# Kernel tuning notes

Hardware: AMD Instinct MI355X
Metric: run time of the kernel (lower is better)

The kernel has to match this reference:

```python
import jax, jax.numpy as jnp
import numpy as np

N_ATOMS = 128
BATCH = 512


def _build_buffers(n):
    # Segments: all non-adjacent bond pairs (i,i+1,j,j+1), j >= i+2, j+1 <= n-1.
    segs = np.array([(i, i + 1, j, j + 1)
                     for i in range(n - 3)
                     for j in range(i + 2, n - 1)], dtype=np.int32)  # (S,4)

    def pidx(a, b):  # linear index of pair (a,b), a<b, in row-major triu(offset=1) order
        return a * n - a * (a + 1) // 2 + (b - a - 1)

    # Each writhe value scatters into its 4 incident residue pairs.
    # Pairs (0,1) [triu idx 0] and (n-2,n-1) [last triu idx] are never incident,
    # so ranks among interior pairs are (triu idx - 1); they are re-inserted by pad.
    inc = []
    for (i, _, j, _) in segs:
        for (a, b) in ((i, j), (i, j + 1), (i + 1, j), (i + 1, j + 1)):
            inc.append(pidx(a, b) - 1)
    indices = np.array(inc, dtype=np.int32)  # (4*S,)

    # Sort permutation placing [upper-triu values, lower-triu values] into
    # row-major order of all off-diagonal (r,c) entries, keyed by r*n + c.
    iu = np.stack(np.triu_indices(n, 1))  # (2, P) row-major
    vals = np.concatenate([iu[0] * n + iu[1], iu[1] * n + iu[0]])
    sort = np.argsort(vals).astype(np.int32)  # (n^2 - n,)
    return segs, indices, sort


def setup_inputs() -> dict:
    key = jax.random.key(0)
    xyz = jax.random.normal(key, (BATCH, N_ATOMS, 3), dtype=jnp.float32)
    segs, indices, sort = _build_buffers(N_ATOMS)
    return {
        "xyz": xyz,
        "segments": jnp.asarray(segs),
        "indices": jnp.asarray(indices),
        "sort": jnp.asarray(sort),
    }


def _divnorm(x):
    return x / jnp.linalg.norm(x, axis=-1, keepdims=True)


def _writhe(xyz, segments):
    # xyz: (B,N,3); segments: (S,4) -> writhe per segment pair, (B,S)
    B, S = xyz.shape[0], segments.shape[0]
    p = xyz[:, segments]  # (B,S,4,3) gathered endpoints [s1a,s1b,s2a,s2b]
    # d[k] = normalize(p_{2+j} - p_i), k = 2*i + j  (the 4 inter-segment directions)
    d = _divnorm((p[:, :, None, 2:, :] - p[:, :, :2, None, :]).reshape(B, S, 4, 3))
    axial = jnp.cross(p[:, :, 3] - p[:, :, 2], p[:, :, 1] - p[:, :, 0])  # (B,S,3)
    signs = jnp.sign(jnp.sum(axial * d[:, :, 0], -1))  # (B,S)
    # 4 face normals of the spherical quadrilateral, then Gauss-Bonnet angle sum
    nrm = _divnorm(jnp.cross(d[:, :, jnp.array([0, 1, 3, 2])],
                             d[:, :, jnp.array([1, 3, 2, 0])]))  # (B,S,4,3)
    cosang = jnp.clip(jnp.sum(nrm * nrm[:, :, jnp.array([1, 2, 3, 0])], -1), -1.0, 1.0)
    omega = jnp.arcsin(cosang).sum(-1)  # (B,S)
    return omega * signs / (2.0 * jnp.pi)


def _laplacian(wr, indices, sort, n):
    # wr: (B,S); scatter-add each writhe into its 4 incident residue pairs,
    # pad back the two untouched pairs, symmetrize, and sort into row-major
    # off-diagonal order -> (B, n^2 - n)
    M = (n * n - n) // 2 - 2
    triu = jnp.zeros((wr.shape[0], M), wr.dtype).at[:, indices].add(
        jnp.repeat(wr, 4, axis=1))
    padded = jnp.pad(triu, ((0, 0), (1, 1)))
    return jnp.concatenate([padded, padded], axis=1)[:, sort]


def reference(xyz, segments, indices, sort):
    xyz = xyz.reshape(-1, N_ATOMS, 3)
    wr = _writhe(xyz, segments)
    return _laplacian(wr, indices, sort, N_ATOMS)
```

## Files before the change

kernel.cpp:

```cpp
#include <hip/hip_runtime.h>
#include <math.h>

#define NATOMS    128
#define NSEG      7875
#define NSEG_PAD  8192
#define OUT_PER_B 16256
#define BLOCK     512
#define TBLOCK    512
#define SIDX_BYTES 16384
#define WS_NEED   (SIDX_BYTES + OUT_PER_B * 8)
#define ZSLOT_OFF (NSEG_PAD * 4)

typedef float v2f __attribute__((ext_vector_type(2)));
__device__ __forceinline__ v2f mk2(float a, float b) { v2f r; r.x = a; r.y = b; return r; }

struct P3 { v2f x, y, z; };
__device__ __forceinline__ P3 psub(P3 a, P3 b) { return {a.x - b.x, a.y - b.y, a.z - b.z}; }
__device__ __forceinline__ P3 pcross(P3 a, P3 b) {
    return {a.y * b.z - a.z * b.y, a.z * b.x - a.x * b.z, a.x * b.y - a.y * b.x};
}
__device__ __forceinline__ v2f pdot(P3 a, P3 b) { return a.x * b.x + a.y * b.y + a.z * b.z; }
__device__ __forceinline__ v2f prsq(v2f q) {
    v2f r; r.x = __builtin_amdgcn_rsqf(q.x); r.y = __builtin_amdgcn_rsqf(q.y); return r;
}
__device__ __forceinline__ v2f pclip1(v2f x) {
    return __builtin_elementwise_min(__builtin_elementwise_max(x, mk2(-1.f, -1.f)),
                                     mk2(1.f, 1.f));
}

__device__ __forceinline__ v2f fast_asin2(v2f x) {
    v2f a = __builtin_elementwise_abs(x);
    v2f p = mk2(-0.0187293f, -0.0187293f);
    p = p * a + mk2( 0.0742610f,  0.0742610f);
    p = p * a + mk2(-0.2121144f, -0.2121144f);
    p = p * a + mk2( 1.5707288f,  1.5707288f);
    v2f om = mk2(1.0f, 1.0f) - a;
    v2f sq; sq.x = __builtin_amdgcn_sqrtf(om.x); sq.y = __builtin_amdgcn_sqrtf(om.y);
    v2f r = mk2(1.57079632679f, 1.57079632679f) - sq * p;
    return __builtin_elementwise_copysign(r, x);
}

__device__ __forceinline__ int seg_row_base(int i) { return 125 * i - (__umul24(i, i - 1) >> 1); }

__device__ __forceinline__ void seed_ij(int s, int &i, int &j) {
    i = (int)((251.0f - __builtin_amdgcn_sqrtf(63001.0f - 8.0f * (float)s)) * 0.5f);
    i = max(i, 0);
    i += (seg_row_base(i + 1) <= s);
    i += (seg_row_base(i + 1) <= s);
    i -= (seg_row_base(i) > s);
    i -= (seg_row_base(i) > s);
    j = s - seg_row_base(i) + i + 2;
}

__device__ __forceinline__ P3 pack3(const float4 &a, const float4 &b) {
    return { mk2(a.x, b.x), mk2(a.y, b.y), mk2(a.z, b.z) };
}

__device__ __forceinline__ v2f seg_writhe_pair(unsigned pa, unsigned pb,
                                               const float4* sp4) {
    int jA = (int)(pa & 127u), iA = (int)(pa >> 7);
    int jB = (int)(pb & 127u), iB = (int)(pb >> 7);

    float4 A0 = sp4[iA], A1 = sp4[iA + 1], A2 = sp4[jA], A3 = sp4[jA + 1];
    float4 B0 = sp4[iB], B1 = sp4[iB + 1], B2 = sp4[jB], B3 = sp4[jB + 1];

    P3 p0 = pack3(A0, B0);
    P3 p1 = pack3(A1, B1);
    P3 p2 = pack3(A2, B2);
    P3 p3 = pack3(A3, B3);

    P3 u0 = psub(p2, p0);
    P3 u1 = psub(p3, p0);
    P3 u2 = psub(p2, p1);
    P3 u3 = psub(p3, p1);

    P3 n0 = pcross(u0, u1);
    P3 n1 = pcross(u1, u3);
    P3 n2 = pcross(u3, u2);
    P3 n3 = pcross(u2, u0);

    v2f q0 = pdot(n0, n0);
    v2f q1 = pdot(n1, n1);
    v2f q2 = pdot(n2, n2);
    v2f q3 = pdot(n3, n3);

    v2f c0 = pclip1(pdot(n0, n1) * prsq(q0 * q1));
    v2f c1 = pclip1(pdot(n1, n2) * prsq(q1 * q2));
    v2f c2 = pclip1(pdot(n2, n3) * prsq(q2 * q3));
    v2f c3 = pclip1(pdot(n3, n0) * prsq(q3 * q0));

    v2f sd = pdot(n2, u0);
    v2f omega = fast_asin2(c0) + fast_asin2(c1) + fast_asin2(c2) + fast_asin2(c3);

    v2f sgn;
    sgn.x = (sd.x > 0.f) ? -1.f : ((sd.x < 0.f) ? 1.f : 0.f);
    sgn.y = (sd.y > 0.f) ? -1.f : ((sd.y < 0.f) ? 1.f : 0.f);

    return omega * sgn * mk2(0.15915494309189535f, 0.15915494309189535f);
}

__global__ __launch_bounds__(TBLOCK) void build_tables(
    unsigned short* __restrict__ gseg,
    uint2*          __restrict__ ptab)
{
    const int tid = blockIdx.x * TBLOCK + threadIdx.x;

    if (tid < NSEG_PAD) {
        int i, j;
        if (tid < NSEG) { seed_ij(tid, i, j); }
        else            { i = 124; j = 126; }
        gseg[tid] = (unsigned short)((i << 7) | j);
    } else {
        const int k = tid - NSEG_PAD;
        if (k < OUT_PER_B) {
            const int r = (int)(((unsigned)k * 132105u) >> 24);
            int c = k - r * 127;
            c += (c >= r);
            const int a  = min(r, c);
            const int bb = max(r, c);

            const int am1 = a - 1;
            const int s00 = 125 * am1 - ((am1 * (am1 - 1)) >> 1) + bb - a - 2;
            const int s10 = s00 + 125 - a;

            const bool v00 = (a >= 1) && (a <= 125) && (bb >= a + 2);
            const bool v01 = (a >= 1) && (a <= 125) && (bb <= 126);
            const bool v10 = (a <= 124) && (bb >= a + 3);
            const bool v11 = (a <= 124) && (bb <= 126) && (bb >= a + 2);

            const unsigned o00 = v00 ? (unsigned)(s00 << 2)       : (unsigned)ZSLOT_OFF;
            const unsigned o01 = v01 ? (unsigned)((s00 + 1) << 2) : (unsigned)ZSLOT_OFF;
            const unsigned o10 = v10 ? (unsigned)(s10 << 2)       : (unsigned)ZSLOT_OFF;
            const unsigned o11 = v11 ? (unsigned)((s10 + 1) << 2) : (unsigned)ZSLOT_OFF;

            ptab[k] = make_uint2(o00 | (o01 << 16), o10 | (o11 << 16));
        }
    }
}

__global__ __launch_bounds__(BLOCK, 2) void writhe_main(
    const float*          __restrict__ xyz,
    const unsigned short* __restrict__ gseg,
    const uint2*          __restrict__ ptab,
    float*                __restrict__ out)
{
    __shared__ float4 sp4[NATOMS];
    __shared__ float  swr[NSEG_PAD + 1];

    const int b = blockIdx.x;
    const int t = threadIdx.x;

    if (t < 3 * NATOMS) {
        float v = xyz[(size_t)b * (3 * NATOMS) + t];
        int a = t / 3, c = t - 3 * a;
        ((float*)&sp4[a])[c] = v;
    }
    if (t == 0) swr[NSEG_PAD] = 0.0f;
    __syncthreads();

    #pragma unroll
    for (int g = 0; g < 4; ++g) {
        const int sA = g * 2048 + t;
        v2f w1 = seg_writhe_pair(gseg[sA],        gseg[sA + 512],  sp4);
        v2f w2 = seg_writhe_pair(gseg[sA + 1024], gseg[sA + 1536], sp4);
        swr[sA]        = w1.x;
        swr[sA + 512]  = w1.y;
        swr[sA + 1024] = w2.x;
        swr[sA + 1536] = w2.y;
    }
    __syncthreads();

    float* ob = out + (size_t)b * OUT_PER_B;
    const char* swb = (const char*)swr;
    for (int k = t; k < OUT_PER_B; k += BLOCK) {
        const uint2 e = ptab[k];
        const float s0 = *(const float*)(swb + (e.x & 0xFFFFu));
        const float s1 = *(const float*)(swb + (e.x >> 16));
        const float s2 = *(const float*)(swb + (e.y & 0xFFFFu));
        const float s3 = *(const float*)(swb + (e.y >> 16));
        __builtin_nontemporal_store(s0 + s1 + s2 + s3, ob + k);
    }
}

__global__ __launch_bounds__(BLOCK, 2) void writhe_fused(
    const float* __restrict__ xyz, float* __restrict__ out)
{
    __shared__ float4 sp4[NATOMS];
    __shared__ float  swr[NSEG_PAD];
    __shared__ unsigned short sidx[NSEG_PAD];
    const int b = blockIdx.x;
    const int t = threadIdx.x;
    if (t < 3 * NATOMS) {
        float v = xyz[(size_t)b * (3 * NATOMS) + t];
        int a = t / 3, c = t - 3 * a;
        ((float*)&sp4[a])[c] = v;
    }
    {
        int s = t * 16;
        if (s < NSEG) {
            int i, j; seed_ij(s, i, j);
            #pragma unroll
            for (int k = 0; k < 16; ++k) {
                if (s < NSEG) sidx[s] = (unsigned short)((i << 7) | j);
                ++s; ++j;
                if (j > 126) { ++i; j = i + 2; }
            }
        }
        if (t < NSEG_PAD - NSEG) sidx[NSEG + t] = (unsigned short)((124 << 7) | 126);
    }
    __syncthreads();
    #pragma unroll
    for (int g = 0; g < 4; ++g) {
        const int sA = g * 2048 + t;
        v2f w1 = seg_writhe_pair(sidx[sA],        sidx[sA + 512],  sp4);
        v2f w2 = seg_writhe_pair(sidx[sA + 1024], sidx[sA + 1536], sp4);
        swr[sA]        = w1.x;
        swr[sA + 512]  = w1.y;
        swr[sA + 1024] = w2.x;
        swr[sA + 1536] = w2.y;
    }
    __syncthreads();
    float* ob = out + (size_t)b * OUT_PER_B;
    for (int k = t; k < OUT_PER_B; k += BLOCK) {
        const int r = (int)(((unsigned)k * 132105u) >> 24);
        int c = k - r * 127;
        c += (c >= r);
        const int a  = min(r, c);
        const int bb = max(r, c);
        const int am1 = a - 1;
        const int s00 = 125 * am1 - ((am1 * (am1 - 1)) >> 1) + bb - a - 2;
        const int s10 = s00 + 125 - a;
        const bool v00 = (a >= 1) && (a <= 125) && (bb >= a + 2);
        const bool v01 = (a >= 1) && (a <= 125) && (bb <= 126);
        const bool v10 = (a <= 124) && (bb >= a + 3);
        const bool v11 = (a <= 124) && (bb <= 126) && (bb >= a + 2);
        const int c00 = min(max(s00,     0), NSEG - 1);
        const int c01 = min(max(s00 + 1, 0), NSEG - 1);
        const int c10 = min(max(s10,     0), NSEG - 1);
        const int c11 = min(max(s10 + 1, 0), NSEG - 1);
        float sum = (v00 ? swr[c00] : 0.0f) + (v01 ? swr[c01] : 0.0f)
                  + (v10 ? swr[c10] : 0.0f) + (v11 ? swr[c11] : 0.0f);
        __builtin_nontemporal_store(sum, ob + k);
    }
}

extern "C" void kernel_launch(void* const* d_in, const int* in_sizes, int n_in,
                              void* d_out, int out_size, void* d_ws, size_t ws_size,
                              hipStream_t stream) {
    const float* xyz = (const float*)d_in[0];
    float*       out = (float*)d_out;

    int B = in_sizes[0] / (NATOMS * 3);

    if (d_ws != nullptr && ws_size >= (size_t)WS_NEED) {
        unsigned short* gseg = (unsigned short*)d_ws;
        uint2*          ptab = (uint2*)((char*)d_ws + SIDX_BYTES);
        const int tgrid = (NSEG_PAD + OUT_PER_B + TBLOCK - 1) / TBLOCK;
        build_tables<<<tgrid, TBLOCK, 0, stream>>>(gseg, ptab);
        writhe_main<<<B, BLOCK, 0, stream>>>(xyz, gseg, ptab, out);
    } else {
        writhe_fused<<<B, BLOCK, 0, stream>>>(xyz, out);
    }
}
```

Measured before the change: 88.19 us.

## Process four consecutive segments per chunk, sharing cross products across neighbours

The writhe phase now assigns each thread chunks of up to four consecutive j segments within a row i. Directions and the shared face normal m[k] are computed once per j and reused by adjacent segments, cutting the cross products, dot products and LDS loads per segment. The scatter table shrinks to one packed 32-bit word per output, holding two base indices plus validity masks, which lowers global table reads in the output phase. Register pressure rises from the five-element arrays, and chunk padding leaves some lanes idle.

```diff
diff --git a/kernel.cpp b/kernel.cpp
--- a/kernel.cpp
+++ b/kernel.cpp
@@ -7,9 +7,9 @@
 #define OUT_PER_B 16256
 #define BLOCK     512
 #define TBLOCK    512
-#define SIDX_BYTES 16384
-#define WS_NEED   (SIDX_BYTES + OUT_PER_B * 8)
-#define ZSLOT_OFF (NSEG_PAD * 4)
+#define NCHUNK    2048
+#define CHUNK_BYTES (NCHUNK * 4)
+#define WS_NEED   (CHUNK_BYTES + OUT_PER_B * 4)
 
 typedef float v2f __attribute__((ext_vector_type(2)));
 __device__ __forceinline__ v2f mk2(float a, float b) { v2f r; r.x = a; r.y = b; return r; }
@@ -56,62 +56,31 @@
     return { mk2(a.x, b.x), mk2(a.y, b.y), mk2(a.z, b.z) };
 }
 
-__device__ __forceinline__ v2f seg_writhe_pair(unsigned pa, unsigned pb,
-                                               const float4* sp4) {
-    int jA = (int)(pa & 127u), iA = (int)(pa >> 7);
-    int jB = (int)(pb & 127u), iB = (int)(pb >> 7);
-
-    float4 A0 = sp4[iA], A1 = sp4[iA + 1], A2 = sp4[jA], A3 = sp4[jA + 1];
-    float4 B0 = sp4[iB], B1 = sp4[iB + 1], B2 = sp4[jB], B3 = sp4[jB + 1];
-
-    P3 p0 = pack3(A0, B0);
-    P3 p1 = pack3(A1, B1);
-    P3 p2 = pack3(A2, B2);
-    P3 p3 = pack3(A3, B3);
-
-    P3 u0 = psub(p2, p0);
-    P3 u1 = psub(p3, p0);
-    P3 u2 = psub(p2, p1);
-    P3 u3 = psub(p3, p1);
-
-    P3 n0 = pcross(u0, u1);
-    P3 n1 = pcross(u1, u3);
-    P3 n2 = pcross(u3, u2);
-    P3 n3 = pcross(u2, u0);
-
-    v2f q0 = pdot(n0, n0);
-    v2f q1 = pdot(n1, n1);
-    v2f q2 = pdot(n2, n2);
-    v2f q3 = pdot(n3, n3);
-
-    v2f c0 = pclip1(pdot(n0, n1) * prsq(q0 * q1));
-    v2f c1 = pclip1(pdot(n1, n2) * prsq(q1 * q2));
-    v2f c2 = pclip1(pdot(n2, n3) * prsq(q2 * q3));
-    v2f c3 = pclip1(pdot(n3, n0) * prsq(q3 * q0));
-
-    v2f sd = pdot(n2, u0);
-    v2f omega = fast_asin2(c0) + fast_asin2(c1) + fast_asin2(c2) + fast_asin2(c3);
-
-    v2f sgn;
-    sgn.x = (sd.x > 0.f) ? -1.f : ((sd.x < 0.f) ? 1.f : 0.f);
-    sgn.y = (sd.y > 0.f) ? -1.f : ((sd.y < 0.f) ? 1.f : 0.f);
-
-    return omega * sgn * mk2(0.15915494309189535f, 0.15915494309189535f);
-}
-
 __global__ __launch_bounds__(TBLOCK) void build_tables(
-    unsigned short* __restrict__ gseg,
-    uint2*          __restrict__ ptab)
+    unsigned* __restrict__ gchunk,
+    unsigned* __restrict__ ptab)
 {
     const int tid = blockIdx.x * TBLOCK + threadIdx.x;
 
-    if (tid < NSEG_PAD) {
-        int i, j;
-        if (tid < NSEG) { seed_ij(tid, i, j); }
-        else            { i = 124; j = 126; }
-        gseg[tid] = (unsigned short)((i << 7) | j);
+    if (tid < NCHUNK) {
+        int c = tid, acc = 0;
+        int i = 0, j0 = 2, s0 = 0, nv = 0;
+        for (int r = 0; r < 125; ++r) {
+            const int len = 125 - r;
+            const int nch = (len + 3) >> 2;
+            if (c >= acc && c < acc + nch) {
+                const int off = (c - acc) << 2;
+                i  = r;
+                j0 = r + 2 + off;
+                s0 = seg_row_base(r) + off;
+                nv = min(4, len - off);
+            }
+            acc += nch;
+        }
+        gchunk[tid] = (unsigned)s0 | ((unsigned)j0 << 13)
+                    | ((unsigned)i << 20) | ((unsigned)nv << 27);
     } else {
-        const int k = tid - NSEG_PAD;
+        const int k = tid - NCHUNK;
         if (k < OUT_PER_B) {
             const int r = (int)(((unsigned)k * 132105u) >> 24);
             int c = k - r * 127;
@@ -128,24 +97,25 @@
             const bool v10 = (a <= 124) && (bb >= a + 3);
             const bool v11 = (a <= 124) && (bb <= 126) && (bb >= a + 2);
 
-            const unsigned o00 = v00 ? (unsigned)(s00 << 2)       : (unsigned)ZSLOT_OFF;
-            const unsigned o01 = v01 ? (unsigned)((s00 + 1) << 2) : (unsigned)ZSLOT_OFF;
-            const unsigned o10 = v10 ? (unsigned)(s10 << 2)       : (unsigned)ZSLOT_OFF;
-            const unsigned o11 = v11 ? (unsigned)((s10 + 1) << 2) : (unsigned)ZSLOT_OFF;
-
-            ptab[k] = make_uint2(o00 | (o01 << 16), o10 | (o11 << 16));
+            const int base0 = v00 ? s00 : (v01 ? s00 + 1 : 0);
+            const int base1 = v10 ? s10 : (v11 ? s10 + 1 : 0);
+            const unsigned m0 = ((v00 || v01) ? 1u : 0u) | ((v00 && v01) ? 2u : 0u);
+            const unsigned m1 = ((v10 || v11) ? 1u : 0u) | ((v10 && v11) ? 2u : 0u);
+
+            ptab[k] = (unsigned)base0 | ((unsigned)base1 << 13)
+                    | (m0 << 26) | (m1 << 28);
         }
     }
 }
 
 __global__ __launch_bounds__(BLOCK, 2) void writhe_main(
-    const float*          __restrict__ xyz,
-    const unsigned short* __restrict__ gseg,
-    const uint2*          __restrict__ ptab,
-    float*                __restrict__ out)
+    const float*    __restrict__ xyz,
+    const unsigned* __restrict__ gchunk,
+    const unsigned* __restrict__ ptab,
+    float*          __restrict__ out)
 {
     __shared__ float4 sp4[NATOMS];
-    __shared__ float  swr[NSEG_PAD + 1];
+    __shared__ float  swr[NSEG_PAD];
 
     const int b = blockIdx.x;
     const int t = threadIdx.x;
@@ -155,31 +125,117 @@
         int a = t / 3, c = t - 3 * a;
         ((float*)&sp4[a])[c] = v;
     }
-    if (t == 0) swr[NSEG_PAD] = 0.0f;
     __syncthreads();
 
     #pragma unroll
-    for (int g = 0; g < 4; ++g) {
-        const int sA = g * 2048 + t;
-        v2f w1 = seg_writhe_pair(gseg[sA],        gseg[sA + 512],  sp4);
-        v2f w2 = seg_writhe_pair(gseg[sA + 1024], gseg[sA + 1536], sp4);
-        swr[sA]        = w1.x;
-        swr[sA + 512]  = w1.y;
-        swr[sA + 1024] = w2.x;
-        swr[sA + 1536] = w2.y;
+    for (int h = 0; h < 2; ++h) {
+        const unsigned eA = gchunk[t + h * 1024];
+        const unsigned eB = gchunk[t + h * 1024 + 512];
+
+        const int s0A = (int)(eA & 0x1FFFu), j0A = (int)((eA >> 13) & 0x7Fu);
+        const int iA  = (int)((eA >> 20) & 0x7Fu), nvA = (int)(eA >> 27);
+        const int s0B = (int)(eB & 0x1FFFu), j0B = (int)((eB >> 13) & 0x7Fu);
+        const int iB  = (int)((eB >> 20) & 0x7Fu), nvB = (int)(eB >> 27);
+
+        const float4 A0 = sp4[iA], A1 = sp4[iA + 1];
+        const float4 B0 = sp4[iB], B1 = sp4[iB + 1];
+        const P3 p0 = pack3(A0, B0);
+        const P3 p1 = pack3(A1, B1);
+
+        v2f va_x[5], va_y[5], va_z[5];
+        v2f vb_x[5], vb_y[5], vb_z[5];
+        P3  m[5];
+        v2f qm[5];
+
+        #pragma unroll
+        for (int k = 0; k < 5; ++k) {
+            const float4 Ak = sp4[min(j0A + k, NATOMS - 1)];
+            const float4 Bk = sp4[min(j0B + k, NATOMS - 1)];
+            const P3 pk = pack3(Ak, Bk);
+            const P3 va = psub(pk, p0);
+            const P3 vb = psub(pk, p1);
+            va_x[k] = va.x; va_y[k] = va.y; va_z[k] = va.z;
+            vb_x[k] = vb.x; vb_y[k] = vb.y; vb_z[k] = vb.z;
+            m[k]  = pcross(va, vb);
+            qm[k] = pdot(m[k], m[k]);
+        }
+
+        #pragma unroll
+        for (int s = 0; s < 4; ++s) {
+            const P3 u0 = {va_x[s],     va_y[s],     va_z[s]};
+            const P3 u1 = {va_x[s + 1], va_y[s + 1], va_z[s + 1]};
+            const P3 u2 = {vb_x[s],     vb_y[s],     vb_z[s]};
+            const P3 u3 = {vb_x[s + 1], vb_y[s + 1], vb_z[s + 1]};
+
+            const P3 n0 = pcross(u0, u1);
+            const P3 n2 = pcross(u3, u2);
+            const P3 n1 = m[s + 1];
+
+            const v2f q0 = pdot(n0, n0);
+            const v2f q1 = qm[s + 1];
+            const v2f q2 = pdot(n2, n2);
+            const v2f q3 = qm[s];
+
+            const v2f c0 = pclip1(pdot(n0, n1) * prsq(q0 * q1));
+            const v2f c1 = pclip1(pdot(n1, n2) * prsq(q1 * q2));
+            const v2f c2 = pclip1((-pdot(n2, m[s])) * prsq(q2 * q3));
+            const v2f c3 = pclip1((-pdot(m[s], n0)) * prsq(q3 * q0));
+
+            const v2f sd = pdot(n2, u0);
+            const v2f omega = fast_asin2(c0) + fast_asin2(c1)
+                            + fast_asin2(c2) + fast_asin2(c3);
+
+            v2f sgn;
+            sgn.x = (sd.x > 0.f) ? -1.f : ((sd.x < 0.f) ? 1.f : 0.f);
+            sgn.y = (sd.y > 0.f) ? -1.f : ((sd.y < 0.f) ? 1.f : 0.f);
+
+            const v2f w = omega * sgn * mk2(0.15915494309189535f, 0.15915494309189535f);
+
+            if (s < nvA) swr[s0A + s] = w.x;
+            if (s < nvB) swr[s0B + s] = w.y;
+        }
     }
     __syncthreads();
 
     float* ob = out + (size_t)b * OUT_PER_B;
-    const char* swb = (const char*)swr;
     for (int k = t; k < OUT_PER_B; k += BLOCK) {
-        const uint2 e = ptab[k];
-        const float s0 = *(const float*)(swb + (e.x & 0xFFFFu));
-        const float s1 = *(const float*)(swb + (e.x >> 16));
-        const float s2 = *(const float*)(swb + (e.y & 0xFFFFu));
-        const float s3 = *(const float*)(swb + (e.y >> 16));
-        __builtin_nontemporal_store(s0 + s1 + s2 + s3, ob + k);
-    }
+        const unsigned e = ptab[k];
+        const int s0 = (int)(e & 0x1FFFu);
+        const int s1 = (int)((e >> 13) & 0x1FFFu);
+        const unsigned vm = e >> 26;
+
+        const float* b0 = &swr[s0];
+        const float* b1 = &swr[s1];
+        const float a0 = b0[0], a1 = b0[1];
+        const float c0 = b1[0], c1 = b1[1];
+
+        const float sum = ((vm & 1u) ? a0 : 0.f) + ((vm & 2u) ? a1 : 0.f)
+                        + ((vm & 4u) ? c0 : 0.f) + ((vm & 8u) ? c1 : 0.f);
+
+        __builtin_nontemporal_store(sum, ob + k);
+    }
+}
+
+__device__ __forceinline__ v2f seg_writhe_pair(unsigned pa, unsigned pb,
+                                               const float4* sp4) {
+    int jA = (int)(pa & 127u), iA = (int)(pa >> 7);
+    int jB = (int)(pb & 127u), iB = (int)(pb >> 7);
+    float4 A0 = sp4[iA], A1 = sp4[iA + 1], A2 = sp4[jA], A3 = sp4[jA + 1];
+    float4 B0 = sp4[iB], B1 = sp4[iB + 1], B2 = sp4[jB], B3 = sp4[jB + 1];
+    P3 p0 = pack3(A0, B0), p1 = pack3(A1, B1), p2 = pack3(A2, B2), p3 = pack3(A3, B3);
+    P3 u0 = psub(p2, p0), u1 = psub(p3, p0), u2 = psub(p2, p1), u3 = psub(p3, p1);
+    P3 n0 = pcross(u0, u1), n1 = pcross(u1, u3), n2 = pcross(u3, u2), n3 = pcross(u2, u0);
+    v2f q0 = pdot(n0, n0), q1 = pdot(n1, n1), q2 = pdot(n2, n2), q3 = pdot(n3, n3);
+    v2f c0 = pclip1(pdot(n0, n1) * prsq(q0 * q1));
+    v2f c1 = pclip1(pdot(n1, n2) * prsq(q1 * q2));
+    v2f c2 = pclip1(pdot(n2, n3) * prsq(q2 * q3));
+    v2f c3 = pclip1(pdot(n3, n0) * prsq(q3 * q0));
+    v2f sd = pdot(n2, u0);
+    v2f omega = fast_asin2(c0) + fast_asin2(c1) + fast_asin2(c2) + fast_asin2(c3);
+    v2f sgn;
+    sgn.x = (sd.x > 0.f) ? -1.f : ((sd.x < 0.f) ? 1.f : 0.f);
+    sgn.y = (sd.y > 0.f) ? -1.f : ((sd.y < 0.f) ? 1.f : 0.f);
+    return omega * sgn * mk2(0.15915494309189535f, 0.15915494309189535f);
 }
 
 __global__ __launch_bounds__(BLOCK, 2) void writhe_fused(
@@ -253,11 +309,11 @@
     int B = in_sizes[0] / (NATOMS * 3);
 
     if (d_ws != nullptr && ws_size >= (size_t)WS_NEED) {
-        unsigned short* gseg = (unsigned short*)d_ws;
-        uint2*          ptab = (uint2*)((char*)d_ws + SIDX_BYTES);
-        const int tgrid = (NSEG_PAD + OUT_PER_B + TBLOCK - 1) / TBLOCK;
-        build_tables<<<tgrid, TBLOCK, 0, stream>>>(gseg, ptab);
-        writhe_main<<<B, BLOCK, 0, stream>>>(xyz, gseg, ptab, out);
+        unsigned* gchunk = (unsigned*)d_ws;
+        unsigned* ptab   = (unsigned*)((char*)d_ws + CHUNK_BYTES);
+        const int tgrid = (NCHUNK + OUT_PER_B + TBLOCK - 1) / TBLOCK;
+        build_tables<<<tgrid, TBLOCK, 0, stream>>>(gchunk, ptab);
+        writhe_main<<<B, BLOCK, 0, stream>>>(xyz, gchunk, ptab, out);
     } else {
         writhe_fused<<<B, BLOCK, 0, stream>>>(xyz, out);
     }
```

After: 96.26 us. 1.09x slower.
